# Kernel tuning notes

Measured on AMD Instinct MI355X. Metric: run time of the kernel, lower is better.

## Reference

```python
import jax, jax.numpy as jnp
import numpy as np

N = 200_000   # occupied voxels
G = 100
C = 128


def _kernel_maps():
    """Build Minkowski-style kernel maps for a 3x3x3 stride-1 sparse conv.
    Returns in_idx, out_idx of shape [27, N] (int32), padded with
    in=0 / out=N sentinel (row N of the scatter buffer is dropped)."""
    rng = np.random.default_rng(0)
    lin = rng.choice(G ** 3, size=N, replace=False)
    coords = np.stack(np.unravel_index(lin, (G, G, G)), axis=1).astype(np.int64)  # [N,3]
    lut = np.full(G ** 3, -1, np.int64)
    lut[lin] = np.arange(N)
    offs = np.array([[dx, dy, dz] for dx in (-1, 0, 1)
                     for dy in (-1, 0, 1) for dz in (-1, 0, 1)], np.int64)
    in_idx = np.zeros((27, N), np.int32)
    out_idx = np.full((27, N), N, np.int32)
    for k, off in enumerate(offs):
        nb = coords + off
        valid = np.all((nb >= 0) & (nb < G), axis=1)
        nb_lin = (nb[:, 0] * G + nb[:, 1]) * G + nb[:, 2]
        j = np.where(valid, lut[np.clip(nb_lin, 0, G ** 3 - 1)], -1)
        sel = np.nonzero(j >= 0)[0]
        m = sel.size
        in_idx[k, :m] = j[sel].astype(np.int32)
        out_idx[k, :m] = sel.astype(np.int32)
    return jnp.asarray(in_idx), jnp.asarray(out_idx)


def setup_inputs() -> dict:
    key = jax.random.key(0)
    ks = jax.random.split(key, 8)
    in_idx, out_idx = _kernel_maps()
    s = 0.02
    return {
        "x_F": jax.random.normal(ks[0], (N, C), jnp.float32),
        "xg_F": jax.random.normal(ks[1], (N, C), jnp.float32),
        "W0": jax.random.normal(ks[2], (27, C, C), jnp.float32) * s,
        "b0": jax.random.normal(ks[3], (C,), jnp.float32) * s,
        "W1": jax.random.normal(ks[4], (27, C, C), jnp.float32) * s,
        "b1": jax.random.normal(ks[5], (C,), jnp.float32) * s,
        "W2": jax.random.normal(ks[6], (27, 2 * C, C), jnp.float32) * s,
        "b2": jax.random.normal(ks[7], (C,), jnp.float32) * s,
        "in_idx": in_idx,
        "out_idx": out_idx,
    }


def _sparse_conv(feat, W, b, in_idx, out_idx):
    # gather-matmul-scatter over the 27 kernel offsets
    n = feat.shape[0]
    cout = W.shape[-1]
    out = jnp.zeros((n + 1, cout), feat.dtype)  # row n is the pad sink
    for k in range(W.shape[0]):
        out = out.at[out_idx[k]].add(feat[in_idx[k]] @ W[k])
    return out[:n] + b


def reference(x_F, xg_F, W0, b0, W1, b1, W2, b2, in_idx, out_idx):
    h = _sparse_conv(xg_F, W0, b0, in_idx, out_idx)          # conv0
    h = jax.nn.relu(_sparse_conv(h, W1, b1, in_idx, out_idx))  # relu(conv1(.))
    cat = jnp.concatenate([x_F, h], axis=1)                   # [N, 2C]
    return _sparse_conv(cat, W2, b2, in_idx, out_idx)         # conv2
```

## Files before the change

kernel.cpp:

```cpp
#include <hip/hip_runtime.h>

#define NV   200000
#define CC   128
#define KOFF 27

typedef unsigned short u16;
typedef __attribute__((ext_vector_type(4))) float f32x4;
typedef __attribute__((ext_vector_type(8))) short bf16x8;

__device__ __forceinline__ u16 f2bf(float f) {
    unsigned u = __float_as_uint(f);
    u += 0x7fffu + ((u >> 16) & 1u);
    return (u16)(u >> 16);
}

#define GLOAD16(gp, lp)                                                        \
    __builtin_amdgcn_global_load_lds(                                          \
        (const __attribute__((address_space(1))) void*)(gp),                   \
        (__attribute__((address_space(3))) void*)(lp), 16, 0, 0)

__global__ void gmap_kernel(const int* __restrict__ iin,
                            const int* __restrict__ iout,
                            int* __restrict__ gmap) {
    int t = blockIdx.x * 256 + threadIdx.x;
    if (t >= KOFF * NV) return;
    int o = iout[t];
    if (o < NV) {
        int k = t / NV;
        gmap[k * NV + o] = iin[t];
    }
}

__global__ void cvt_kernel(const float* __restrict__ src,
                           u16* __restrict__ dst, int n4) {
    int i = blockIdx.x * 256 + threadIdx.x;
    if (i >= n4) return;
    float4 v = ((const float4*)src)[i];
    ushort4 o;
    o.x = f2bf(v.x); o.y = f2bf(v.y); o.z = f2bf(v.z); o.w = f2bf(v.w);
    ((ushort4*)dst)[i] = o;
}

__global__ void packw_kernel(const float* __restrict__ W,
                             u16* __restrict__ Wp, int cin, int total) {
    int t = blockIdx.x * 256 + threadIdx.x;
    if (t >= total) return;
    int j  = t & 7;
    int l  = (t >> 3) & 63;
    int cf = (t >> 9) & 7;
    int sk = t >> 12;
    int nks = cin >> 5;
    int k  = sk / nks;
    int ks = sk - k * nks;
    int kpos = ks * 32 + (l >> 4) * 8 + j;
    int col  = cf * 16 + (l & 15);
    Wp[t] = f2bf(W[((size_t)k * cin + kpos) * CC + col]);
}

template <int NKS, int ACT, int OUT16>
__global__ __launch_bounds__(256, 2)
void conv_kernel(const u16* __restrict__ f0, const u16* __restrict__ f1,
                 const u16* __restrict__ Wp, const float* __restrict__ bias,
                 const int* __restrict__ gmap, const u16* __restrict__ zrow,
                 float* __restrict__ out32, u16* __restrict__ out16) {
    constexpr int NSTEP = KOFF * NKS;

    __shared__ u16 Ab[2][512 * 8];
    __shared__ u16 Bb[2][8][64][8];

    const int tid = threadIdx.x;
    const int l   = tid & 63;
    const int w   = tid >> 6;
    const int wr  = w >> 1, wc = w & 1;
    const int r0  = blockIdx.x * 128;

    const int qA  = (l & 3) ^ ((l >> 2) & 3);
    const int rA0 = 32 * w + (l >> 2);
    const int rA1 = rA0 + 16;

    float bcol[4];
#pragma unroll
    for (int c = 0; c < 4; ++c) bcol[c] = bias[wc * 64 + c * 16 + (l & 15)];

    f32x4 acc[4][4] = {};

    int gA, gB;
    auto loadGmap = [&](int s) {
        int k = s / NKS;
        int ra = r0 + rA0, rb = r0 + rA1;
        gA = (ra < NV) ? gmap[k * NV + ra] : -1;
        gB = (rb < NV) ? gmap[k * NV + rb] : -1;
    };

    auto stage = [&](int s, int buf) {
        int k = s / NKS, ks = s - k * NKS;
        const u16* base;
        int slice;
        if constexpr (NKS == 8) {
            base  = (ks < 4) ? f0 : f1;
            slice = (ks & 3) * 32;
        } else {
            base  = f0;
            slice = ks * 32;
        }
        const u16* sA0 = (gA >= 0) ? base + (size_t)gA * CC + slice + qA * 8
                                   : zrow + qA * 8;
        const u16* sA1 = (gB >= 0) ? base + (size_t)gB * CC + slice + qA * 8
                                   : zrow + qA * 8;
        GLOAD16(sA0, &Ab[buf][(2 * w) * 64 * 8]);
        GLOAD16(sA1, &Ab[buf][(2 * w + 1) * 64 * 8]);
        const u16* wsrc = Wp + (((size_t)(k * NKS + ks) * 8 + 2 * w) * 512) + l * 8;
        GLOAD16(wsrc,       &Bb[buf][2 * w][0][0]);
        GLOAD16(wsrc + 512, &Bb[buf][2 * w + 1][0][0]);
    };

    auto compute = [&](int buf) {
        bf16x8 a[4], b[4];
        const int q = l >> 4;
#pragma unroll
        for (int rf = 0; rf < 4; ++rf) {
            int rl = wr * 64 + rf * 16 + (l & 15);
            int ci = rl * 4 + (q ^ (rl & 3));
            a[rf] = *(const bf16x8*)&Ab[buf][ci * 8];
        }
#pragma unroll
        for (int c = 0; c < 4; ++c)
            b[c] = *(const bf16x8*)&Bb[buf][wc * 4 + c][l][0];
#pragma unroll
        for (int rf = 0; rf < 4; ++rf)
#pragma unroll
            for (int c = 0; c < 4; ++c)
                acc[rf][c] = __builtin_amdgcn_mfma_f32_16x16x32_bf16(
                    a[rf], b[c], acc[rf][c], 0, 0, 0);
    };

    loadGmap(0);
    stage(0, 0);
    loadGmap(1);
    __syncthreads();

    int cur = 0;
    for (int s = 0; s < NSTEP; ++s) {
        if (s + 1 < NSTEP) {
            stage(s + 1, cur ^ 1);
            if (s + 2 < NSTEP) loadGmap(s + 2);
        }
        compute(cur);
        __syncthreads();
        cur ^= 1;
    }

#pragma unroll
    for (int rf = 0; rf < 4; ++rf) {
        int rbase = r0 + wr * 64 + rf * 16 + (l >> 4) * 4;
#pragma unroll
        for (int i = 0; i < 4; ++i) {
            int row = rbase + i;
            if (row < NV) {
#pragma unroll
                for (int c = 0; c < 4; ++c) {
                    float v = acc[rf][c][i] + bcol[c];
                    if constexpr (ACT) v = fmaxf(v, 0.f);
                    int col = wc * 64 + c * 16 + (l & 15);
                    if constexpr (OUT16) out16[(size_t)row * CC + col] = f2bf(v);
                    else                 out32[(size_t)row * CC + col] = v;
                }
            }
        }
    }
}

extern "C" void kernel_launch(void* const* d_in, const int* in_sizes, int n_in,
                              void* d_out, int out_size, void* d_ws, size_t ws_size,
                              hipStream_t stream) {
    (void)in_sizes; (void)n_in; (void)out_size; (void)ws_size;
    const float* xF  = (const float*)d_in[0];
    const float* xgF = (const float*)d_in[1];
    const float* W0  = (const float*)d_in[2];
    const float* b0  = (const float*)d_in[3];
    const float* W1  = (const float*)d_in[4];
    const float* b1  = (const float*)d_in[5];
    const float* W2  = (const float*)d_in[6];
    const float* b2  = (const float*)d_in[7];
    const int* iin   = (const int*)d_in[8];
    const int* iout  = (const int*)d_in[9];
    float* out = (float*)d_out;
    char* ws = (char*)d_ws;

    size_t off = 0;
    int* gmap  = (int*)(ws + off);  off += (size_t)KOFF * NV * 4;
    u16* zrow  = (u16*)(ws + off);  off += 256;
    u16* F0    = (u16*)(ws + off);  off += (size_t)NV * CC * 2;
    u16* F1    = (u16*)(ws + off);  off += (size_t)NV * CC * 2;
    u16* F2    = (u16*)(ws + off);  off += (size_t)NV * CC * 2;
    u16* WP0   = (u16*)(ws + off);  off += (size_t)KOFF * 128 * 128 * 2;
    u16* WP1   = (u16*)(ws + off);  off += (size_t)KOFF * 128 * 128 * 2;
    u16* WP2   = (u16*)(ws + off);  off += (size_t)KOFF * 256 * 128 * 2;

    (void)hipMemsetAsync(gmap, 0xFF, (size_t)KOFF * NV * 4, stream);
    (void)hipMemsetAsync(zrow, 0, 256, stream);

    gmap_kernel<<<(KOFF * NV + 255) / 256, 256, 0, stream>>>(iin, iout, gmap);
    cvt_kernel<<<(NV * CC / 4 + 255) / 256, 256, 0, stream>>>(xgF, F0, NV * CC / 4);
    cvt_kernel<<<(NV * CC / 4 + 255) / 256, 256, 0, stream>>>(xF,  F2, NV * CC / 4);
    packw_kernel<<<(KOFF * 128 * 128 + 255) / 256, 256, 0, stream>>>(W0, WP0, 128, KOFF * 128 * 128);
    packw_kernel<<<(KOFF * 128 * 128 + 255) / 256, 256, 0, stream>>>(W1, WP1, 128, KOFF * 128 * 128);
    packw_kernel<<<(KOFF * 256 * 128 + 255) / 256, 256, 0, stream>>>(W2, WP2, 256, KOFF * 256 * 128);

    const int NB = (NV + 127) / 128;
    conv_kernel<4, 0, 1><<<NB, 256, 0, stream>>>(F0, F0, WP0, b0, gmap, zrow, nullptr, F1);
    conv_kernel<4, 1, 1><<<NB, 256, 0, stream>>>(F1, F1, WP1, b1, gmap, zrow, nullptr, F0);
    conv_kernel<8, 0, 0><<<NB, 256, 0, stream>>>(F2, F0, WP2, b2, gmap, zrow, out, nullptr);
}
```

Measured before the change: 789.5 us.

## Restructure sparse conv to 256-row tiles with triple-buffered 64-wide K pipeline

Each conv block now covers 256 rows with 512 threads (8 waves, each computing 64x64) and K steps 64 channels at a time instead of 32. A three-stage LDS ring replaces double buffering, with manual vmcnt waits and raw s_barrier calls. Gather indices are prefetched through inline-asm loads two steps ahead. MFMA sections are wrapped in s_setprio. The aim is to halve the number of barrier and sync steps, amortize weight loads over more rows, and keep more gathers in flight. The cost is about 3x LDS per block (roughly 144KB), which likely limits occupancy to one block per CU. The hand-counted vmcnt values are fragile and must stay exactly in step with the issued loads.

```diff
diff --git a/kernel.cpp b/kernel.cpp
--- a/kernel.cpp
+++ b/kernel.cpp
@@ -18,6 +18,13 @@
     __builtin_amdgcn_global_load_lds(                                          \
         (const __attribute__((address_space(1))) void*)(gp),                   \
         (__attribute__((address_space(3))) void*)(lp), 16, 0, 0)
+
+#define WAITV(n)                                                               \
+    do {                                                                       \
+        asm volatile("s_waitcnt vmcnt(" #n ")" ::: "memory");                  \
+        __builtin_amdgcn_sched_barrier(0);                                     \
+    } while (0)
+#define BARRIER() asm volatile("s_barrier" ::: "memory")
 
 __global__ void gmap_kernel(const int* __restrict__ iin,
                             const int* __restrict__ iout,
@@ -57,111 +64,148 @@
     Wp[t] = f2bf(W[((size_t)k * cin + kpos) * CC + col]);
 }
 
-template <int NKS, int ACT, int OUT16>
-__global__ __launch_bounds__(256, 2)
+template <int NKT, int ACT, int OUT16>
+__global__ __launch_bounds__(512, 2)
 void conv_kernel(const u16* __restrict__ f0, const u16* __restrict__ f1,
                  const u16* __restrict__ Wp, const float* __restrict__ bias,
                  const int* __restrict__ gmap, const u16* __restrict__ zrow,
                  float* __restrict__ out32, u16* __restrict__ out16) {
-    constexpr int NSTEP = KOFF * NKS;
-
-    __shared__ u16 Ab[2][512 * 8];
-    __shared__ u16 Bb[2][8][64][8];
+    constexpr int NT = KOFF * NKT;
+
+    __shared__ u16 Ab[3][256 * 64];
+    __shared__ u16 Bb[3][16 * 512];
 
     const int tid = threadIdx.x;
     const int l   = tid & 63;
     const int w   = tid >> 6;
     const int wr  = w >> 1, wc = w & 1;
-    const int r0  = blockIdx.x * 128;
-
-    const int qA  = (l & 3) ^ ((l >> 2) & 3);
-    const int rA0 = 32 * w + (l >> 2);
-    const int rA1 = rA0 + 16;
+    const int r0  = blockIdx.x * 256;
+
+    const int lrow8 = l >> 3;
+    const int csw   = (l & 7) ^ lrow8;
+    const u16* zsrc = zrow + csw * 8;
+
+    int rowIdx[4];
+#pragma unroll
+    for (int i = 0; i < 4; ++i) rowIdx[i] = r0 + i * 64 + w * 8 + lrow8;
 
     float bcol[4];
 #pragma unroll
-    for (int c = 0; c < 4; ++c) bcol[c] = bias[wc * 64 + c * 16 + (l & 15)];
+    for (int n = 0; n < 4; ++n) bcol[n] = bias[wc * 64 + n * 16 + (l & 15)];
 
     f32x4 acc[4][4] = {};
 
-    int gA, gB;
-    auto loadGmap = [&](int s) {
-        int k = s / NKS;
-        int ra = r0 + rA0, rb = r0 + rA1;
-        gA = (ra < NV) ? gmap[k * NV + ra] : -1;
-        gB = (rb < NV) ? gmap[k * NV + rb] : -1;
+    int gmA[4], gmB[4];
+    auto loadGm = [&](int t, int* gm) {
+        int k = t / NKT;
+        const int* base = gmap + (size_t)k * NV;
+#pragma unroll
+        for (int i = 0; i < 4; ++i) {
+            const int* p = base + rowIdx[i];
+            asm volatile("global_load_dword %0, %1, off"
+                         : "=v"(gm[i]) : "v"(p) : "memory");
+        }
     };
 
-    auto stage = [&](int s, int buf) {
-        int k = s / NKS, ks = s - k * NKS;
-        const u16* base;
-        int slice;
-        if constexpr (NKS == 8) {
-            base  = (ks < 4) ? f0 : f1;
-            slice = (ks & 3) * 32;
+    auto stage = [&](int t, int buf, const int* gm) {
+        int k = t / NKT, kt = t % NKT;
+        const u16* fb;
+        int coloff;
+        if constexpr (NKT == 4) {
+            fb = (kt < 2) ? f0 : f1;  coloff = (kt & 1) * 64;
         } else {
-            base  = f0;
-            slice = ks * 32;
-        }
-        const u16* sA0 = (gA >= 0) ? base + (size_t)gA * CC + slice + qA * 8
-                                   : zrow + qA * 8;
-        const u16* sA1 = (gB >= 0) ? base + (size_t)gB * CC + slice + qA * 8
-                                   : zrow + qA * 8;
-        GLOAD16(sA0, &Ab[buf][(2 * w) * 64 * 8]);
-        GLOAD16(sA1, &Ab[buf][(2 * w + 1) * 64 * 8]);
-        const u16* wsrc = Wp + (((size_t)(k * NKS + ks) * 8 + 2 * w) * 512) + l * 8;
-        GLOAD16(wsrc,       &Bb[buf][2 * w][0][0]);
-        GLOAD16(wsrc + 512, &Bb[buf][2 * w + 1][0][0]);
+            fb = f0;                  coloff = kt * 64;
+        }
+#pragma unroll
+        for (int i = 0; i < 4; ++i) {
+            int g = gm[i];
+            const u16* src = (g >= 0)
+                ? fb + ((size_t)g << 7) + coloff + csw * 8 : zsrc;
+            GLOAD16(src, &Ab[buf][(i * 64 + w * 8) * 64]);
+        }
+        const u16* wsrc = Wp + ((size_t)(k * (2 * NKT) + kt * 2) * 8) * 512 + l * 8;
+        GLOAD16(wsrc + (size_t)w * 512,       &Bb[buf][w * 512]);
+        GLOAD16(wsrc + (size_t)(8 + w) * 512, &Bb[buf][(8 + w) * 512]);
     };
 
     auto compute = [&](int buf) {
-        bf16x8 a[4], b[4];
-        const int q = l >> 4;
-#pragma unroll
-        for (int rf = 0; rf < 4; ++rf) {
-            int rl = wr * 64 + rf * 16 + (l & 15);
-            int ci = rl * 4 + (q ^ (rl & 3));
-            a[rf] = *(const bf16x8*)&Ab[buf][ci * 8];
-        }
-#pragma unroll
-        for (int c = 0; c < 4; ++c)
-            b[c] = *(const bf16x8*)&Bb[buf][wc * 4 + c][l][0];
-#pragma unroll
-        for (int rf = 0; rf < 4; ++rf)
-#pragma unroll
-            for (int c = 0; c < 4; ++c)
-                acc[rf][c] = __builtin_amdgcn_mfma_f32_16x16x32_bf16(
-                    a[rf], b[c], acc[rf][c], 0, 0, 0);
+        bf16x8 a[2][4], b[2][4];
+#pragma unroll
+        for (int ks = 0; ks < 2; ++ks) {
+#pragma unroll
+            for (int m = 0; m < 4; ++m) {
+                int row = wr * 64 + m * 16 + (l & 15);
+                int ch  = (ks * 4 + (l >> 4)) ^ (row & 7);
+                a[ks][m] = *(const bf16x8*)&Ab[buf][row * 64 + ch * 8];
+            }
+#pragma unroll
+            for (int n = 0; n < 4; ++n)
+                b[ks][n] = *(const bf16x8*)&Bb[buf][(ks * 8 + wc * 4 + n) * 512 + l * 8];
+        }
+        __builtin_amdgcn_s_setprio(1);
+#pragma unroll
+        for (int ks = 0; ks < 2; ++ks)
+#pragma unroll
+            for (int m = 0; m < 4; ++m)
+#pragma unroll
+                for (int n = 0; n < 4; ++n)
+                    acc[m][n] = __builtin_amdgcn_mfma_f32_16x16x32_bf16(
+                        a[ks][m], b[ks][n], acc[m][n], 0, 0, 0);
+        __builtin_amdgcn_s_setprio(0);
     };
 
-    loadGmap(0);
-    stage(0, 0);
-    loadGmap(1);
-    __syncthreads();
-
-    int cur = 0;
-    for (int s = 0; s < NSTEP; ++s) {
-        if (s + 1 < NSTEP) {
-            stage(s + 1, cur ^ 1);
-            if (s + 2 < NSTEP) loadGmap(s + 2);
-        }
-        compute(cur);
-        __syncthreads();
-        cur ^= 1;
+    loadGm(0, gmA);
+    WAITV(0);
+    loadGm(1, gmB);
+    stage(0, 0, gmA);
+    WAITV(6);
+    loadGm(2, gmA);
+    stage(1, 1, gmB);
+
+    int cur = 0, sb = 2;
+    for (int tp = 0; tp < NT; tp += 2) {
+        {
+            int t = tp;
+            if (t + 2 < NT) {
+                WAITV(6);
+                if (t + 3 < NT) loadGm(t + 3, gmB);
+                stage(t + 2, sb, gmA);
+            } else if (t + 1 < NT) { WAITV(6); }
+            else                   { WAITV(0); }
+            BARRIER();
+            compute(cur);
+            BARRIER();
+            cur = (cur == 2) ? 0 : cur + 1;
+            sb  = (sb  == 2) ? 0 : sb  + 1;
+        }
+        {
+            int t = tp + 1;
+            if (t + 2 < NT) {
+                WAITV(6);
+                if (t + 3 < NT) loadGm(t + 3, gmA);
+                stage(t + 2, sb, gmB);
+            } else if (t + 1 < NT) { WAITV(6); }
+            else                   { WAITV(0); }
+            BARRIER();
+            compute(cur);
+            BARRIER();
+            cur = (cur == 2) ? 0 : cur + 1;
+            sb  = (sb  == 2) ? 0 : sb  + 1;
+        }
     }
 
 #pragma unroll
-    for (int rf = 0; rf < 4; ++rf) {
-        int rbase = r0 + wr * 64 + rf * 16 + (l >> 4) * 4;
+    for (int m = 0; m < 4; ++m) {
+        int rbase = r0 + wr * 64 + m * 16 + (l >> 4) * 4;
 #pragma unroll
         for (int i = 0; i < 4; ++i) {
             int row = rbase + i;
             if (row < NV) {
 #pragma unroll
-                for (int c = 0; c < 4; ++c) {
-                    float v = acc[rf][c][i] + bcol[c];
+                for (int n = 0; n < 4; ++n) {
+                    float v = acc[m][n][i] + bcol[n];
                     if constexpr (ACT) v = fmaxf(v, 0.f);
-                    int col = wc * 64 + c * 16 + (l & 15);
+                    int col = wc * 64 + n * 16 + (l & 15);
                     if constexpr (OUT16) out16[(size_t)row * CC + col] = f2bf(v);
                     else                 out32[(size_t)row * CC + col] = v;
                 }
@@ -188,7 +232,7 @@
     char* ws = (char*)d_ws;
 
     size_t off = 0;
-    int* gmap  = (int*)(ws + off);  off += (size_t)KOFF * NV * 4;
+    int* gmap  = (int*)(ws + off);  off += ((size_t)KOFF * NV + 512) * 4;
     u16* zrow  = (u16*)(ws + off);  off += 256;
     u16* F0    = (u16*)(ws + off);  off += (size_t)NV * CC * 2;
     u16* F1    = (u16*)(ws + off);  off += (size_t)NV * CC * 2;
@@ -197,7 +241,7 @@
     u16* WP1   = (u16*)(ws + off);  off += (size_t)KOFF * 128 * 128 * 2;
     u16* WP2   = (u16*)(ws + off);  off += (size_t)KOFF * 256 * 128 * 2;
 
-    (void)hipMemsetAsync(gmap, 0xFF, (size_t)KOFF * NV * 4, stream);
+    (void)hipMemsetAsync(gmap, 0xFF, ((size_t)KOFF * NV + 512) * 4, stream);
     (void)hipMemsetAsync(zrow, 0, 256, stream);
 
     gmap_kernel<<<(KOFF * NV + 255) / 256, 256, 0, stream>>>(iin, iout, gmap);
@@ -207,8 +251,8 @@
     packw_kernel<<<(KOFF * 128 * 128 + 255) / 256, 256, 0, stream>>>(W1, WP1, 128, KOFF * 128 * 128);
     packw_kernel<<<(KOFF * 256 * 128 + 255) / 256, 256, 0, stream>>>(W2, WP2, 256, KOFF * 256 * 128);
 
-    const int NB = (NV + 127) / 128;
-    conv_kernel<4, 0, 1><<<NB, 256, 0, stream>>>(F0, F0, WP0, b0, gmap, zrow, nullptr, F1);
-    conv_kernel<4, 1, 1><<<NB, 256, 0, stream>>>(F1, F1, WP1, b1, gmap, zrow, nullptr, F0);
-    conv_kernel<8, 0, 0><<<NB, 256, 0, stream>>>(F2, F0, WP2, b2, gmap, zrow, out, nullptr);
-}
+    const int NB = (NV + 255) / 256;
+    conv_kernel<2, 0, 1><<<NB, 512, 0, stream>>>(F0, F0, WP0, b0, gmap, zrow, nullptr, F1);
+    conv_kernel<2, 1, 1><<<NB, 512, 0, stream>>>(F1, F1, WP1, b1, gmap, zrow, nullptr, F0);
+    conv_kernel<4, 0, 0><<<NB, 512, 0, stream>>>(F2, F0, WP2, b2, gmap, zrow, out, nullptr);
+}
```

Result: slower. 1.155 ms (+46.3%).
